# Kernel tuning notes

Measured on AMD Instinct MI355X. Metric: run time of the kernel, lower is better.

The kernel has to match this reference:

```python
import jax, jax.numpy as jnp
import numpy as np

B, SEQ_LEN, N_VARS, N_MARK = 16, 96, 862, 4
D_MODEL, D_STATE, D_CONV, D_FF = 512, 16, 2, 512
DT_RANK = 32  # ceil(d_model/16)
E_LAYERS = 2
PRED_LEN = 96
EPS = 1e-5


def _layer_norm(x, w, b):
    mu = x.mean(-1, keepdims=True)
    var = ((x - mu) ** 2).mean(-1, keepdims=True)
    return (x - mu) / jnp.sqrt(var + EPS) * w + b


def _selective_scan(xc, dt, Bm, Cm, A, D):
    # xc, dt: [B,S,d]; Bm, Cm: [B,S,ds]; A: [d,ds]; D: [d]
    def step(h, inp):
        x_t, dt_t, B_t, C_t = inp  # [B,d],[B,d],[B,ds],[B,ds]
        dA = jnp.exp(dt_t[..., None] * A)                      # [B,d,ds]
        h = dA * h + (dt_t * x_t)[..., None] * B_t[:, None, :]
        return h, jnp.einsum('bds,bs->bd', h, C_t)
    h0 = jnp.zeros((xc.shape[0], A.shape[0], A.shape[1]), xc.dtype)
    xs = tuple(jnp.swapaxes(t, 0, 1) for t in (xc, dt, Bm, Cm))
    _, ys = jax.lax.scan(step, h0, xs)
    return jnp.swapaxes(ys, 0, 1) + xc * D


def _mamba(x, in_W, conv_W, conv_b, xproj_W, dt_W, dt_b, A_log, D, out_W):
    d = in_W.shape[0] // 2
    xz = x @ in_W.T                                             # [B,S,2d]
    xi, z = xz[..., :d], xz[..., d:]
    xp = jnp.pad(xi, ((0, 0), (1, 0), (0, 0)))                  # causal pad, d_conv=2
    xc = xp[:, :-1] * conv_W[:, 0] + xp[:, 1:] * conv_W[:, 1] + conv_b
    xc = jax.nn.silu(xc)
    dbc = xc @ xproj_W.T                                        # [B,S,dt_rank+2*ds]
    dtr = dbc[..., :DT_RANK]
    Bm = dbc[..., DT_RANK:DT_RANK + D_STATE]
    Cm = dbc[..., DT_RANK + D_STATE:]
    dt = jax.nn.softplus(dtr @ dt_W.T + dt_b)
    A = -jnp.exp(A_log)
    y = _selective_scan(xc, dt, Bm, Cm, A, D)
    return (y * jax.nn.silu(z)) @ out_W.T


def _forward(x_enc, x_mark_enc, emb_W, emb_b,
             mf_in_W, mf_conv_W, mf_conv_b, mf_xproj_W, mf_dt_W, mf_dt_b, mf_A_log, mf_D, mf_out_W,
             mr_in_W, mr_conv_W, mr_conv_b, mr_xproj_W, mr_dt_W, mr_dt_b, mr_A_log, mr_D, mr_out_W,
             conv1_W, conv1_b, conv2_W, conv2_b, ln1_w, ln1_b, ln2_w, ln2_b,
             enc_norm_w, enc_norm_b, proj_W, proj_b):
    # RevIN-style instance normalization over time
    means = x_enc.mean(1, keepdims=True)
    xe = x_enc - means
    stdev = jnp.sqrt(jnp.mean(xe ** 2, axis=1, keepdims=True) + EPS)  # unbiased=False
    xe = xe / stdev
    N = x_enc.shape[2]
    # inverted embedding: variates (+ time marks) are tokens, Linear over time axis
    tok = jnp.concatenate([jnp.swapaxes(xe, 1, 2), jnp.swapaxes(x_mark_enc, 1, 2)], axis=1)
    x = tok @ emb_W.T + emb_b                                   # [B, N+4, d_model]
    for l in range(E_LAYERS):
        fwd = _mamba(x, mf_in_W[l], mf_conv_W[l], mf_conv_b[l], mf_xproj_W[l],
                     mf_dt_W[l], mf_dt_b[l], mf_A_log[l], mf_D[l], mf_out_W[l])
        rev = _mamba(x[:, ::-1], mr_in_W[l], mr_conv_W[l], mr_conv_b[l], mr_xproj_W[l],
                     mr_dt_W[l], mr_dt_b[l], mr_A_log[l], mr_D[l], mr_out_W[l])[:, ::-1]
        x = x + fwd + rev
        y = x = _layer_norm(x, ln1_w[l], ln1_b[l])
        y = jax.nn.relu(y @ conv1_W[l].T + conv1_b[l])          # 1x1 conv == linear
        y = y @ conv2_W[l].T + conv2_b[l]
        x = _layer_norm(x + y, ln2_w[l], ln2_b[l])
    x = _layer_norm(x, enc_norm_w, enc_norm_b)
    dec = jnp.swapaxes(x @ proj_W.T + proj_b, 1, 2)[:, :, :N]   # [B, pred_len, N]
    dec = dec * stdev[:, 0][:, None, :] + means[:, 0][:, None, :]
    return dec


def setup_inputs() -> dict:
    key = jax.random.key(0)
    ks = iter(jax.random.split(key, 64))
    nrm = lambda shape, s=0.02: jax.random.normal(next(ks), shape, jnp.float32) * s
    inp = {
        'x_enc': jax.random.normal(next(ks), (B, SEQ_LEN, N_VARS), jnp.float32),
        'x_mark_enc': jax.random.normal(next(ks), (B, SEQ_LEN, N_MARK), jnp.float32),
        'x_dec': jnp.zeros((1, 1, 1), jnp.float32),
        'x_mark_dec': jnp.zeros((1, 1, 1), jnp.float32),
        'emb_W': nrm((D_MODEL, SEQ_LEN)),
        'emb_b': jnp.zeros((D_MODEL,), jnp.float32),
    }
    for p in ('mf', 'mr'):
        inp[p + '_in_W'] = nrm((E_LAYERS, 2 * D_MODEL, D_MODEL))
        inp[p + '_conv_W'] = nrm((E_LAYERS, D_MODEL, D_CONV), 0.1)
        inp[p + '_conv_b'] = jnp.zeros((E_LAYERS, D_MODEL), jnp.float32)
        inp[p + '_xproj_W'] = nrm((E_LAYERS, DT_RANK + 2 * D_STATE, D_MODEL))
        inp[p + '_dt_W'] = nrm((E_LAYERS, D_MODEL, DT_RANK), 0.1)
        inp[p + '_dt_b'] = nrm((E_LAYERS, D_MODEL), 0.1)
        inp[p + '_A_log'] = jnp.log(jnp.broadcast_to(
            jnp.arange(1, D_STATE + 1, dtype=jnp.float32), (E_LAYERS, D_MODEL, D_STATE)))
        inp[p + '_D'] = jnp.ones((E_LAYERS, D_MODEL), jnp.float32)
        inp[p + '_out_W'] = nrm((E_LAYERS, D_MODEL, D_MODEL))
    inp['conv1_W'] = nrm((E_LAYERS, D_FF, D_MODEL))
    inp['conv1_b'] = jnp.zeros((E_LAYERS, D_FF), jnp.float32)
    inp['conv2_W'] = nrm((E_LAYERS, D_MODEL, D_FF))
    inp['conv2_b'] = jnp.zeros((E_LAYERS, D_MODEL), jnp.float32)
    inp['ln1_w'] = jnp.ones((E_LAYERS, D_MODEL), jnp.float32)
    inp['ln1_b'] = jnp.zeros((E_LAYERS, D_MODEL), jnp.float32)
    inp['ln2_w'] = jnp.ones((E_LAYERS, D_MODEL), jnp.float32)
    inp['ln2_b'] = jnp.zeros((E_LAYERS, D_MODEL), jnp.float32)
    inp['enc_norm_w'] = jnp.ones((D_MODEL,), jnp.float32)
    inp['enc_norm_b'] = jnp.zeros((D_MODEL,), jnp.float32)
    inp['proj_W'] = nrm((PRED_LEN, D_MODEL))
    inp['proj_b'] = jnp.zeros((PRED_LEN,), jnp.float32)
    return inp


def reference(x_enc, x_mark_enc, x_dec, x_mark_dec, emb_W, emb_b,
              mf_in_W, mf_conv_W, mf_conv_b, mf_xproj_W, mf_dt_W, mf_dt_b, mf_A_log, mf_D, mf_out_W,
              mr_in_W, mr_conv_W, mr_conv_b, mr_xproj_W, mr_dt_W, mr_dt_b, mr_A_log, mr_D, mr_out_W,
              conv1_W, conv1_b, conv2_W, conv2_b, ln1_w, ln1_b, ln2_w, ln2_b,
              enc_norm_w, enc_norm_b, proj_W, proj_b):
    return _forward(x_enc, x_mark_enc, emb_W, emb_b,
                    mf_in_W, mf_conv_W, mf_conv_b, mf_xproj_W, mf_dt_W, mf_dt_b, mf_A_log, mf_D, mf_out_W,
                    mr_in_W, mr_conv_W, mr_conv_b, mr_xproj_W, mr_dt_W, mr_dt_b, mr_A_log, mr_D, mr_out_W,
                    conv1_W, conv1_b, conv2_W, conv2_b, ln1_w, ln1_b, ln2_w, ln2_b,
                    enc_norm_w, enc_norm_b, proj_W, proj_b)
```

## Files before the change

kernel.cpp:

```cpp
#include <hip/hip_runtime.h>
#include <math.h>

#define BATCH   16
#define SEQ     96
#define NVARS   862
#define NMARK   4
#define LTOK    866
#define MROWS   (BATCH*LTOK)
#define DM      512
#define DSTATE  16
#define DTRANK  32
#define DFF     512
#define PRED    96
#define EPS_F   1e-5f

#define CCH     32
#define TCH     28

typedef __attribute__((ext_vector_type(4))) float f32x4;
typedef __attribute__((ext_vector_type(8))) short bf16x8;

#define LDSK 40

__device__ __forceinline__ short f2bf(float f) {
    unsigned u = __builtin_bit_cast(unsigned, f);
    u += 0x7fffu + ((u >> 16) & 1u);
    return (short)(u >> 16);
}

__global__ __launch_bounds__(256) void gemm_mfma(
    const float* __restrict__ A, int lda,
    const float* __restrict__ W,
    const float* __restrict__ bias,
    const float* __restrict__ res,
    float* __restrict__ out, int ldo,
    int M, int N, int K, int rev, int act,
    int final_mode, const float* __restrict__ fstd, const float* __restrict__ fmean)
{
    __shared__ short Als[128 * LDSK];
    __shared__ short Bls[128 * LDSK];
    const int tid  = threadIdx.x;
    const int lane = tid & 63;
    const int wid  = tid >> 6;
    const int wm   = wid >> 1;
    const int wn   = wid & 1;
    const int fr   = lane & 15;
    const int g    = lane >> 4;
    const int m0 = blockIdx.y * 128, n0 = blockIdx.x * 128;

    int    rowq[4], kgq[4];
    size_t aoff[4], woff[4];
    bool   aval[4], wval[4];
#pragma unroll
    for (int q = 0; q < 4; ++q) {
        const int slot = tid + q * 256;
        const int row = slot >> 3, kg = slot & 7;
        rowq[q] = row; kgq[q] = kg;
        const int gm = m0 + row;
        aval[q] = (gm < M);
        int rm = gm;
        if (rev && aval[q]) { int b = gm / LTOK; int t = gm - b * LTOK; rm = b * LTOK + (LTOK - 1 - t); }
        aoff[q] = (size_t)rm * lda + kg * 4;
        const int gn = n0 + row;
        wval[q] = (gn < N);
        woff[q] = (size_t)gn * K + kg * 4;
    }

    f32x4 acc[4][4];
#pragma unroll
    for (int i = 0; i < 4; ++i)
#pragma unroll
        for (int j = 0; j < 4; ++j) { f32x4 z = {0.f, 0.f, 0.f, 0.f}; acc[i][j] = z; }

    for (int k0 = 0; k0 < K; k0 += 32) {
        float4 avq[4], wvq[4];
        const float4 f0 = make_float4(0.f, 0.f, 0.f, 0.f);
#pragma unroll
        for (int q = 0; q < 4; ++q) {
            avq[q] = aval[q] ? *(const float4*)(A + aoff[q] + k0) : f0;
            wvq[q] = wval[q] ? *(const float4*)(W + woff[q] + k0) : f0;
        }
        __syncthreads();
#pragma unroll
        for (int q = 0; q < 4; ++q) {
            short4 sa, sw;
            sa.x = f2bf(avq[q].x); sa.y = f2bf(avq[q].y);
            sa.z = f2bf(avq[q].z); sa.w = f2bf(avq[q].w);
            sw.x = f2bf(wvq[q].x); sw.y = f2bf(wvq[q].y);
            sw.z = f2bf(wvq[q].z); sw.w = f2bf(wvq[q].w);
            *(short4*)&Als[rowq[q] * LDSK + kgq[q] * 4] = sa;
            *(short4*)&Bls[rowq[q] * LDSK + kgq[q] * 4] = sw;
        }
        __syncthreads();

        bf16x8 a4[4], b4[4];
#pragma unroll
        for (int i = 0; i < 4; ++i) {
            a4[i] = *(const bf16x8*)&Als[(wm * 64 + i * 16 + fr) * LDSK + g * 8];
            b4[i] = *(const bf16x8*)&Bls[(wn * 64 + i * 16 + fr) * LDSK + g * 8];
        }
#pragma unroll
        for (int mi = 0; mi < 4; ++mi)
#pragma unroll
            for (int ni = 0; ni < 4; ++ni)
                acc[mi][ni] = __builtin_amdgcn_mfma_f32_16x16x32_bf16(
                    a4[mi], b4[ni], acc[mi][ni], 0, 0, 0);
    }

#pragma unroll
    for (int mi = 0; mi < 4; ++mi) {
#pragma unroll
        for (int ni = 0; ni < 4; ++ni) {
            const int gn = n0 + wn * 64 + ni * 16 + fr;
            if (gn >= N) continue;
#pragma unroll
            for (int j = 0; j < 4; ++j) {
                const int gm = m0 + wm * 64 + mi * 16 + g * 4 + j;
                if (gm >= M) continue;
                float v = acc[mi][ni][j];
                if (bias) v += bias[gn];
                if (act == 1) v = fmaxf(v, 0.f);
                else if (act == 2) v = (v > 20.f) ? v : log1pf(__expf(v));
                if (res) v += res[(size_t)gm * DM + gn];
                if (!final_mode) {
                    out[(size_t)gm * ldo + gn] = v;
                } else {
                    const int bb = gm / LTOK, vv = gm - bb * LTOK;
                    if (vv < NVARS) {
                        out[((size_t)bb * PRED + gn) * NVARS + vv] =
                            v * fstd[bb * NVARS + vv] + fmean[bb * NVARS + vv];
                    }
                }
            }
        }
    }
}

__global__ void stats_kernel(const float* __restrict__ x_enc,
                             float* __restrict__ means, float* __restrict__ stdev)
{
    int i = blockIdx.x * blockDim.x + threadIdx.x;
    if (i >= BATCH * NVARS) return;
    int b = i / NVARS, v = i - b * NVARS;
    const float* p = x_enc + (size_t)b * SEQ * NVARS + v;
    float s = 0.f;
    for (int t = 0; t < SEQ; ++t) s += p[(size_t)t * NVARS];
    float mu = s / (float)SEQ;
    float ss = 0.f;
    for (int t = 0; t < SEQ; ++t) { float d = p[(size_t)t * NVARS] - mu; ss += d * d; }
    means[i] = mu;
    stdev[i] = sqrtf(ss / (float)SEQ + EPS_F);
}

__global__ void tok_kernel(const float* __restrict__ x_enc, const float* __restrict__ x_mark,
                           const float* __restrict__ means, const float* __restrict__ stdev,
                           float* __restrict__ tok)
{
    int i = blockIdx.x * blockDim.x + threadIdx.x;
    if (i >= MROWS * SEQ) return;
    int s = i % SEQ;
    int row = i / SEQ;
    int b = row / LTOK, l = row - b * LTOK;
    float val;
    if (l < NVARS) {
        val = (x_enc[((size_t)b * SEQ + s) * NVARS + l] - means[b * NVARS + l])
              / stdev[b * NVARS + l];
    } else {
        val = x_mark[((size_t)b * SEQ + s) * NMARK + (l - NVARS)];
    }
    tok[i] = val;
}

__global__ void conv_silu_kernel(const float* __restrict__ xz, float* __restrict__ xc,
                                 const float* __restrict__ cW, const float* __restrict__ cb)
{
    int i = blockIdx.x * blockDim.x + threadIdx.x;
    if (i >= MROWS * DM) return;
    int d = i & (DM - 1);
    int row = i >> 9;
    int t = row % LTOK;
    float cur = xz[(size_t)row * 1024 + d];
    float prev = (t == 0) ? 0.f : xz[(size_t)(row - 1) * 1024 + d];
    float v = prev * cW[d * 2 + 0] + cur * cW[d * 2 + 1] + cb[d];
    xc[i] = v * (1.f / (1.f + __expf(-v)));
}

__global__ __launch_bounds__(256) void scan1_kernel(
    const float* __restrict__ xc, const float* __restrict__ dt,
    const float* __restrict__ dbc, const float* __restrict__ A_log,
    float* __restrict__ aprod, float* __restrict__ hpart)
{
    __shared__ float Ls[TCH * 32];
    const int tid = threadIdx.x;
    const int d = blockIdx.x * 256 + tid;
    const int c = blockIdx.y;
    const int b = blockIdx.z;
    const int t0 = c * TCH;
    const int tend = min(t0 + TCH, LTOK);
    const size_t rowb = (size_t)b * LTOK;

    for (int i = tid; i < TCH * 32; i += 256) {
        const int tr = min(t0 + (i >> 5), LTOK - 1);
        Ls[i] = dbc[(rowb + tr) * 64 + 32 + (i & 31)];
    }
    __syncthreads();

    float Ads[16];
#pragma unroll
    for (int s = 0; s < 16; ++s) Ads[s] = -__expf(A_log[d * DSTATE + s]);
    float h[16];
#pragma unroll
    for (int s = 0; s < 16; ++s) h[s] = 0.f;
    float sumdt = 0.f;

    for (int t = t0; t < tend; ++t) {
        const size_t row = rowb + t;
        const float dtv = dt[row * DM + d];
        const float xcv = xc[row * DM + d];
        const float du = dtv * xcv;
        sumdt += dtv;
        const float* Bp = &Ls[(t - t0) * 32];
#pragma unroll
        for (int s = 0; s < 16; ++s) {
            const float dA = __expf(dtv * Ads[s]);
            h[s] = dA * h[s] + du * Bp[s];
        }
    }
#pragma unroll
    for (int s = 0; s < 16; ++s) {
        const size_t oidx = ((size_t)(b * CCH + c) * 16 + s) * DM + d;
        aprod[oidx] = __expf(Ads[s] * sumdt);
        hpart[oidx] = h[s];
    }
}

__global__ __launch_bounds__(256) void scan2_kernel(
    const float* __restrict__ aprod, const float* __restrict__ hpart,
    float* __restrict__ hinit)
{
    const int gid = blockIdx.x * 256 + threadIdx.x;
    const int d = gid & (DM - 1);
    const int s = (gid >> 9) & 15;
    const int b = gid >> 13;
    float h = 0.f;
    for (int c = 0; c < CCH; ++c) {
        const size_t idx = ((size_t)(b * CCH + c) * 16 + s) * DM + d;
        const float ap = aprod[idx];
        const float hp = hpart[idx];
        hinit[idx] = h;
        h = hp + ap * h;
    }
}

__global__ __launch_bounds__(256) void scan3_kernel(
    const float* __restrict__ xc, const float* __restrict__ dt,
    const float* __restrict__ dbc, const float* __restrict__ xz,
    const float* __restrict__ A_log, const float* __restrict__ Dp,
    const float* __restrict__ hinit, float* __restrict__ ym)
{
    __shared__ float Ls[TCH * 32];
    const int tid = threadIdx.x;
    const int d = blockIdx.x * 256 + tid;
    const int c = blockIdx.y;
    const int b = blockIdx.z;
    const int t0 = c * TCH;
    const int tend = min(t0 + TCH, LTOK);
    const size_t rowb = (size_t)b * LTOK;

    for (int i = tid; i < TCH * 32; i += 256) {
        const int tr = min(t0 + (i >> 5), LTOK - 1);
        Ls[i] = dbc[(rowb + tr) * 64 + 32 + (i & 31)];
    }
    __syncthreads();

    float Ads[16];
#pragma unroll
    for (int s = 0; s < 16; ++s) Ads[s] = -__expf(A_log[d * DSTATE + s]);
    float h[16];
#pragma unroll
    for (int s = 0; s < 16; ++s)
        h[s] = hinit[((size_t)(b * CCH + c) * 16 + s) * DM + d];
    const float Dd = Dp[d];

    for (int t = t0; t < tend; ++t) {
        const size_t row = rowb + t;
        const float dtv = dt[row * DM + d];
        const float xcv = xc[row * DM + d];
        const float du = dtv * xcv;
        const float* Bp = &Ls[(t - t0) * 32];
        float p0 = 0.f, p1 = 0.f, p2 = 0.f, p3 = 0.f;
#pragma unroll
        for (int s = 0; s < 16; ++s) {
            const float dA = __expf(dtv * Ads[s]);
            const float hn = dA * h[s] + du * Bp[s];
            h[s] = hn;
            const float pc = hn * Bp[16 + s];
            if ((s & 3) == 0) p0 += pc;
            else if ((s & 3) == 1) p1 += pc;
            else if ((s & 3) == 2) p2 += pc;
            else p3 += pc;
        }
        const float y = (p0 + p1) + (p2 + p3) + xcv * Dd;
        const float z = xz[row * 1024 + DM + d];
        ym[row * DM + d] = y * (z * (1.f / (1.f + __expf(-z))));
    }
}

__global__ __launch_bounds__(256) void ln_kernel(const float* __restrict__ in,
                                                 const float* __restrict__ w,
                                                 const float* __restrict__ bp,
                                                 float* __restrict__ out)
{
    const int row = blockIdx.x;
    const int tid = threadIdx.x;
    const float2 v = *(const float2*)(in + (size_t)row * DM + tid * 2);
    float s  = v.x + v.y;
    float ss = v.x * v.x + v.y * v.y;
    for (int off = 32; off; off >>= 1) {
        s  += __shfl_down(s, off);
        ss += __shfl_down(ss, off);
    }
    __shared__ float sh[10];
    const int wid = tid >> 6, lane = tid & 63;
    if (lane == 0) { sh[wid] = s; sh[4 + wid] = ss; }
    __syncthreads();
    if (tid == 0) {
        float S = sh[0] + sh[1] + sh[2] + sh[3];
        float SS = sh[4] + sh[5] + sh[6] + sh[7];
        float mu = S / (float)DM;
        float var = SS / (float)DM - mu * mu;
        sh[8] = mu; sh[9] = rsqrtf(var + EPS_F);
    }
    __syncthreads();
    const float mu = sh[8], rstd = sh[9];
    const int c = tid * 2;
    float2 o;
    o.x = (v.x - mu) * rstd * w[c]     + bp[c];
    o.y = (v.y - mu) * rstd * w[c + 1] + bp[c + 1];
    *(float2*)(out + (size_t)row * DM + c) = o;
}

static inline void launch_gemm(hipStream_t st, const float* A, int lda, const float* W,
                               const float* bias, const float* res, float* out, int ldo,
                               int M, int N, int K, int rev, int act,
                               int fin = 0, const float* fstd = nullptr, const float* fmean = nullptr)
{
    dim3 g((N + 127) / 128, (M + 127) / 128);
    hipLaunchKernelGGL(gemm_mfma, g, dim3(256), 0, st,
                       A, lda, W, bias, res, out, ldo, M, N, K, rev, act, fin, fstd, fmean);
}

extern "C" void kernel_launch(void* const* d_in, const int* in_sizes, int n_in,
                              void* d_out, int out_size, void* d_ws, size_t ws_size,
                              hipStream_t stream)
{
    const float* x_enc   = (const float*)d_in[0];
    const float* x_mark  = (const float*)d_in[1];
    const float* emb_W   = (const float*)d_in[4];
    const float* emb_b   = (const float*)d_in[5];
    const float* m_in_W[2]    = { (const float*)d_in[6],  (const float*)d_in[15] };
    const float* m_conv_W[2]  = { (const float*)d_in[7],  (const float*)d_in[16] };
    const float* m_conv_b[2]  = { (const float*)d_in[8],  (const float*)d_in[17] };
    const float* m_xproj_W[2] = { (const float*)d_in[9],  (const float*)d_in[18] };
    const float* m_dt_W[2]    = { (const float*)d_in[10], (const float*)d_in[19] };
    const float* m_dt_b[2]    = { (const float*)d_in[11], (const float*)d_in[20] };
    const float* m_A_log[2]   = { (const float*)d_in[12], (const float*)d_in[21] };
    const float* m_D[2]       = { (const float*)d_in[13], (const float*)d_in[22] };
    const float* m_out_W[2]   = { (const float*)d_in[14], (const float*)d_in[23] };
    const float* conv1_W = (const float*)d_in[24];
    const float* conv1_b = (const float*)d_in[25];
    const float* conv2_W = (const float*)d_in[26];
    const float* conv2_b = (const float*)d_in[27];
    const float* ln1_w = (const float*)d_in[28];
    const float* ln1_b = (const float*)d_in[29];
    const float* ln2_w = (const float*)d_in[30];
    const float* ln2_b = (const float*)d_in[31];
    const float* enc_w = (const float*)d_in[32];
    const float* enc_b = (const float*)d_in[33];
    const float* proj_W = (const float*)d_in[34];
    const float* proj_b = (const float*)d_in[35];

    float* ws = (float*)d_ws;
    size_t o = 0;
    float* means = ws + o; o += 13824;
    float* stdev = ws + o; o += 13824;
    float* xbuf  = ws + o; o += (size_t)MROWS * DM;
    float* accb  = ws + o; o += (size_t)MROWS * DM;
    float* xzb   = ws + o; o += (size_t)MROWS * 1024;
    float* xcb   = ws + o; o += (size_t)MROWS * DM;
    float* dtb   = ws + o; o += (size_t)MROWS * DM;
    float* dbcb  = ws + o; o += (size_t)MROWS * 64;
    float* ybuf  = ws + o; o += (size_t)MROWS * DM;
    const size_t NSUM = (size_t)BATCH * CCH * 16 * DM;
    float* aprod = ws + o; o += NSUM;
    float* hpart = ws + o; o += NSUM;
    float* hinit = ws + o; o += NSUM;
    float* tok   = xzb;
    float* hbuf  = xzb;
    float* x2buf = ybuf;

    hipLaunchKernelGGL(stats_kernel, dim3((BATCH * NVARS + 255) / 256), dim3(256), 0, stream,
                       x_enc, means, stdev);
    hipLaunchKernelGGL(tok_kernel, dim3((MROWS * SEQ + 255) / 256), dim3(256), 0, stream,
                       x_enc, x_mark, means, stdev, tok);
    launch_gemm(stream, tok, SEQ, emb_W, emb_b, nullptr, xbuf, DM, MROWS, DM, SEQ, 0, 0);

    for (int l = 0; l < 2; ++l) {
        for (int dir = 0; dir < 2; ++dir) {
            const float* inW  = m_in_W[dir]    + (size_t)l * 2 * DM * DM;
            const float* cW   = m_conv_W[dir]  + (size_t)l * DM * 2;
            const float* cb   = m_conv_b[dir]  + (size_t)l * DM;
            const float* xpW  = m_xproj_W[dir] + (size_t)l * 64 * DM;
            const float* dtW  = m_dt_W[dir]    + (size_t)l * DM * DTRANK;
            const float* dtbias = m_dt_b[dir]  + (size_t)l * DM;
            const float* Alog = m_A_log[dir]   + (size_t)l * DM * DSTATE;
            const float* Dp   = m_D[dir]       + (size_t)l * DM;
            const float* outW = m_out_W[dir]   + (size_t)l * DM * DM;

            launch_gemm(stream, xbuf, DM, inW, nullptr, nullptr, xzb, 1024,
                        MROWS, 2 * DM, DM, dir, 0);
            hipLaunchKernelGGL(conv_silu_kernel, dim3((MROWS * DM + 255) / 256), dim3(256),
                               0, stream, xzb, xcb, cW, cb);
            launch_gemm(stream, xcb, DM, xpW, nullptr, nullptr, dbcb, 64,
                        MROWS, 64, DM, 0, 0);
            launch_gemm(stream, dbcb, 64, dtW, dtbias, nullptr, dtb, DM,
                        MROWS, DM, DTRANK, 0, 2);
            hipLaunchKernelGGL(scan1_kernel, dim3(2, CCH, BATCH), dim3(256), 0, stream,
                               xcb, dtb, dbcb, Alog, aprod, hpart);
            hipLaunchKernelGGL(scan2_kernel, dim3((BATCH * 16 * DM) / 256), dim3(256), 0, stream,
                               aprod, hpart, hinit);
            hipLaunchKernelGGL(scan3_kernel, dim3(2, CCH, BATCH), dim3(256), 0, stream,
                               xcb, dtb, dbcb, xzb, Alog, Dp, hinit, ybuf);
            launch_gemm(stream, ybuf, DM, outW, nullptr, dir == 0 ? xbuf : accb,
                        accb, DM, MROWS, DM, DM, dir, 0);
        }
        hipLaunchKernelGGL(ln_kernel, dim3(MROWS), dim3(256), 0, stream,
                           accb, ln1_w + l * DM, ln1_b + l * DM, x2buf);
        launch_gemm(stream, x2buf, DM, conv1_W + (size_t)l * DFF * DM,
                    conv1_b + l * DFF, nullptr, hbuf, DFF, MROWS, DFF, DM, 0, 1);
        launch_gemm(stream, hbuf, DFF, conv2_W + (size_t)l * DM * DFF,
                    conv2_b + l * DM, x2buf, accb, DM, MROWS, DM, DFF, 0, 0);
        hipLaunchKernelGGL(ln_kernel, dim3(MROWS), dim3(256), 0, stream,
                           accb, ln2_w + l * DM, ln2_b + l * DM, xbuf);
    }

    hipLaunchKernelGGL(ln_kernel, dim3(MROWS), dim3(256), 0, stream,
                       xbuf, enc_w, enc_b, x2buf);
    launch_gemm(stream, x2buf, DM, proj_W, proj_b, nullptr, (float*)d_out, 0,
                MROWS, PRED, DM, 0, 0, 1, stdev, means);
}
```

Baseline: 1.785 ms.

## Store GEMM operands as bf16 and load tiles directly into LDS

```diff
diff --git a/kernel.cpp b/kernel.cpp
--- a/kernel.cpp
+++ b/kernel.cpp
@@ -19,51 +19,57 @@
 
 typedef __attribute__((ext_vector_type(4))) float f32x4;
 typedef __attribute__((ext_vector_type(8))) short bf16x8;
-
-#define LDSK 40
+typedef unsigned short ushort_t;
 
 __device__ __forceinline__ short f2bf(float f) {
     unsigned u = __builtin_bit_cast(unsigned, f);
     u += 0x7fffu + ((u >> 16) & 1u);
     return (short)(u >> 16);
 }
-
-__global__ __launch_bounds__(256) void gemm_mfma(
-    const float* __restrict__ A, int lda,
-    const float* __restrict__ W,
+__device__ __forceinline__ float bf2f(ushort_t u) {
+    return __builtin_bit_cast(float, (unsigned)u << 16);
+}
+
+__device__ __forceinline__ void gl2lds16(const ushort_t* g, ushort_t* l) {
+    __builtin_amdgcn_global_load_lds(
+        (const __attribute__((address_space(1))) unsigned int*)(g),
+        (__attribute__((address_space(3))) unsigned int*)(l),
+        16, 0, 0);
+}
+
+__global__ __launch_bounds__(256) void gemm_bf16(
+    const ushort_t* __restrict__ A, int lda,
+    const ushort_t* __restrict__ W, int ldw,
     const float* __restrict__ bias,
-    const float* __restrict__ res,
-    float* __restrict__ out, int ldo,
-    int M, int N, int K, int rev, int act,
-    int final_mode, const float* __restrict__ fstd, const float* __restrict__ fmean)
-{
-    __shared__ short Als[128 * LDSK];
-    __shared__ short Bls[128 * LDSK];
+    const float* __restrict__ resf, const ushort_t* __restrict__ resb,
+    float* __restrict__ outf, ushort_t* __restrict__ outb, int ldo,
+    int M, int N, int K, int rev, int act, int mode,
+    const float* __restrict__ fstd, const float* __restrict__ fmean)
+{
+    __shared__ ushort_t Als[128 * 32];
+    __shared__ ushort_t Bls[128 * 32];
     const int tid  = threadIdx.x;
     const int lane = tid & 63;
-    const int wid  = tid >> 6;
-    const int wm   = wid >> 1;
-    const int wn   = wid & 1;
-    const int fr   = lane & 15;
-    const int g    = lane >> 4;
+    const int w    = tid >> 6;
+    const int wm   = w >> 1;
+    const int wn   = w & 1;
     const int m0 = blockIdx.y * 128, n0 = blockIdx.x * 128;
 
-    int    rowq[4], kgq[4];
-    size_t aoff[4], woff[4];
-    bool   aval[4], wval[4];
-#pragma unroll
-    for (int q = 0; q < 4; ++q) {
-        const int slot = tid + q * 256;
-        const int row = slot >> 3, kg = slot & 7;
-        rowq[q] = row; kgq[q] = kg;
-        const int gm = m0 + row;
-        aval[q] = (gm < M);
+    size_t asrc[2], wsrc[2];
+    int lbase[2];
+#pragma unroll
+    for (int i = 0; i < 2; ++i) {
+        const int byte = (i * 4 + w) * 1024 + lane * 16;
+        const int row  = byte >> 6;
+        const int c    = (byte >> 4) & 3;
+        const int g    = c ^ ((row >> 1) & 3);
+        int gm = m0 + row; if (gm > M - 1) gm = M - 1;
         int rm = gm;
-        if (rev && aval[q]) { int b = gm / LTOK; int t = gm - b * LTOK; rm = b * LTOK + (LTOK - 1 - t); }
-        aoff[q] = (size_t)rm * lda + kg * 4;
-        const int gn = n0 + row;
-        wval[q] = (gn < N);
-        woff[q] = (size_t)gn * K + kg * 4;
+        if (rev) { int b = gm / LTOK; int t = gm - b * LTOK; rm = b * LTOK + (LTOK - 1 - t); }
+        asrc[i] = (size_t)rm * lda + g * 8;
+        int gn = n0 + row; if (gn > N - 1) gn = N - 1;
+        wsrc[i] = (size_t)gn * ldw + g * 8;
+        lbase[i] = (i * 4 + w) * 512;
     }
 
     f32x4 acc[4][4];
@@ -72,32 +78,23 @@
 #pragma unroll
         for (int j = 0; j < 4; ++j) { f32x4 z = {0.f, 0.f, 0.f, 0.f}; acc[i][j] = z; }
 
+    const int fr = lane & 15;
+    const int kg = lane >> 4;
+    const int cg = kg ^ ((fr >> 1) & 3);
+
     for (int k0 = 0; k0 < K; k0 += 32) {
-        float4 avq[4], wvq[4];
-        const float4 f0 = make_float4(0.f, 0.f, 0.f, 0.f);
-#pragma unroll
-        for (int q = 0; q < 4; ++q) {
-            avq[q] = aval[q] ? *(const float4*)(A + aoff[q] + k0) : f0;
-            wvq[q] = wval[q] ? *(const float4*)(W + woff[q] + k0) : f0;
-        }
         __syncthreads();
-#pragma unroll
-        for (int q = 0; q < 4; ++q) {
-            short4 sa, sw;
-            sa.x = f2bf(avq[q].x); sa.y = f2bf(avq[q].y);
-            sa.z = f2bf(avq[q].z); sa.w = f2bf(avq[q].w);
-            sw.x = f2bf(wvq[q].x); sw.y = f2bf(wvq[q].y);
-            sw.z = f2bf(wvq[q].z); sw.w = f2bf(wvq[q].w);
-            *(short4*)&Als[rowq[q] * LDSK + kgq[q] * 4] = sa;
-            *(short4*)&Bls[rowq[q] * LDSK + kgq[q] * 4] = sw;
-        }
+        gl2lds16(A + asrc[0] + k0, &Als[lbase[0]]);
+        gl2lds16(A + asrc[1] + k0, &Als[lbase[1]]);
+        gl2lds16(W + wsrc[0] + k0, &Bls[lbase[0]]);
+        gl2lds16(W + wsrc[1] + k0, &Bls[lbase[1]]);
         __syncthreads();
 
         bf16x8 a4[4], b4[4];
 #pragma unroll
         for (int i = 0; i < 4; ++i) {
-            a4[i] = *(const bf16x8*)&Als[(wm * 64 + i * 16 + fr) * LDSK + g * 8];
-            b4[i] = *(const bf16x8*)&Bls[(wn * 64 + i * 16 + fr) * LDSK + g * 8];
+            a4[i] = *(const bf16x8*)&Als[(wm * 64 + i * 16 + fr) * 32 + cg * 8];
+            b4[i] = *(const bf16x8*)&Bls[(wn * 64 + i * 16 + fr) * 32 + cg * 8];
         }
 #pragma unroll
         for (int mi = 0; mi < 4; ++mi)
@@ -115,25 +112,44 @@
             if (gn >= N) continue;
 #pragma unroll
             for (int j = 0; j < 4; ++j) {
-                const int gm = m0 + wm * 64 + mi * 16 + g * 4 + j;
+                const int gm = m0 + wm * 64 + mi * 16 + kg * 4 + j;
                 if (gm >= M) continue;
                 float v = acc[mi][ni][j];
                 if (bias) v += bias[gn];
                 if (act == 1) v = fmaxf(v, 0.f);
                 else if (act == 2) v = (v > 20.f) ? v : log1pf(__expf(v));
-                if (res) v += res[(size_t)gm * DM + gn];
-                if (!final_mode) {
-                    out[(size_t)gm * ldo + gn] = v;
+                if (resf) v += resf[(size_t)gm * DM + gn];
+                else if (resb) v += bf2f(resb[(size_t)gm * DM + gn]);
+                if (mode == 0) {
+                    if (outf) outf[(size_t)gm * ldo + gn] = v;
+                    if (outb) outb[(size_t)gm * ldo + gn] = (ushort_t)f2bf(v);
+                } else if (mode == 2) {
+                    if (gn < DM) outf[(size_t)gm * DM + gn] = v;
+                    else         outb[(size_t)gm * DM + gn - DM] = (ushort_t)f2bf(v);
                 } else {
                     const int bb = gm / LTOK, vv = gm - bb * LTOK;
                     if (vv < NVARS) {
-                        out[((size_t)bb * PRED + gn) * NVARS + vv] =
+                        outf[((size_t)bb * PRED + gn) * NVARS + vv] =
                             v * fstd[bb * NVARS + vv] + fmean[bb * NVARS + vv];
                     }
                 }
             }
         }
     }
+}
+
+struct CvtJobs {
+    const float* src[12];
+    ushort_t*    dst[12];
+    int          n[12];
+};
+__global__ void cvt_kernel(CvtJobs jobs) {
+    const int j = blockIdx.y;
+    const float* s = jobs.src[j];
+    ushort_t* d = jobs.dst[j];
+    const int n = jobs.n[j];
+    for (int i = blockIdx.x * blockDim.x + threadIdx.x; i < n; i += gridDim.x * blockDim.x)
+        d[i] = (ushort_t)f2bf(s[i]);
 }
 
 __global__ void stats_kernel(const float* __restrict__ x_enc,
@@ -154,7 +170,7 @@
 
 __global__ void tok_kernel(const float* __restrict__ x_enc, const float* __restrict__ x_mark,
                            const float* __restrict__ means, const float* __restrict__ stdev,
-                           float* __restrict__ tok)
+                           ushort_t* __restrict__ tok)
 {
     int i = blockIdx.x * blockDim.x + threadIdx.x;
     if (i >= MROWS * SEQ) return;
@@ -168,10 +184,11 @@
     } else {
         val = x_mark[((size_t)b * SEQ + s) * NMARK + (l - NVARS)];
     }
-    tok[i] = val;
-}
-
-__global__ void conv_silu_kernel(const float* __restrict__ xz, float* __restrict__ xc,
+    tok[i] = (ushort_t)f2bf(val);
+}
+
+__global__ void conv_silu_kernel(const float* __restrict__ xi, float* __restrict__ xc,
+                                 ushort_t* __restrict__ xc_bf,
                                  const float* __restrict__ cW, const float* __restrict__ cb)
 {
     int i = blockIdx.x * blockDim.x + threadIdx.x;
@@ -179,10 +196,12 @@
     int d = i & (DM - 1);
     int row = i >> 9;
     int t = row % LTOK;
-    float cur = xz[(size_t)row * 1024 + d];
-    float prev = (t == 0) ? 0.f : xz[(size_t)(row - 1) * 1024 + d];
+    float cur = xi[i];
+    float prev = (t == 0) ? 0.f : xi[i - DM];
     float v = prev * cW[d * 2 + 0] + cur * cW[d * 2 + 1] + cb[d];
-    xc[i] = v * (1.f / (1.f + __expf(-v)));
+    float sv = v * (1.f / (1.f + __expf(-v)));
+    xc[i] = sv;
+    xc_bf[i] = (ushort_t)f2bf(sv);
 }
 
 __global__ __launch_bounds__(256) void scan1_kernel(
@@ -235,8 +254,7 @@
 }
 
 __global__ __launch_bounds__(256) void scan2_kernel(
-    const float* __restrict__ aprod, const float* __restrict__ hpart,
-    float* __restrict__ hinit)
+    float* __restrict__ aprod, const float* __restrict__ hpart)
 {
     const int gid = blockIdx.x * 256 + threadIdx.x;
     const int d = gid & (DM - 1);
@@ -247,16 +265,16 @@
         const size_t idx = ((size_t)(b * CCH + c) * 16 + s) * DM + d;
         const float ap = aprod[idx];
         const float hp = hpart[idx];
-        hinit[idx] = h;
+        aprod[idx] = h;
         h = hp + ap * h;
     }
 }
 
 __global__ __launch_bounds__(256) void scan3_kernel(
     const float* __restrict__ xc, const float* __restrict__ dt,
-    const float* __restrict__ dbc, const float* __restrict__ xz,
+    const float* __restrict__ dbc, const ushort_t* __restrict__ zbf,
     const float* __restrict__ A_log, const float* __restrict__ Dp,
-    const float* __restrict__ hinit, float* __restrict__ ym)
+    const float* __restrict__ hinit, ushort_t* __restrict__ ym)
 {
     __shared__ float Ls[TCH * 32];
     const int tid = threadIdx.x;
@@ -301,15 +319,16 @@
             else p3 += pc;
         }
         const float y = (p0 + p1) + (p2 + p3) + xcv * Dd;
-        const float z = xz[row * 1024 + DM + d];
-        ym[row * DM + d] = y * (z * (1.f / (1.f + __expf(-z))));
+        const float z = bf2f(zbf[row * DM + d]);
+        ym[row * DM + d] = (ushort_t)f2bf(y * (z * (1.f / (1.f + __expf(-z)))));
     }
 }
 
 __global__ __launch_bounds__(256) void ln_kernel(const float* __restrict__ in,
                                                  const float* __restrict__ w,
                                                  const float* __restrict__ bp,
-                                                 float* __restrict__ out)
+                                                 float* __restrict__ outf,
+                                                 ushort_t* __restrict__ outb)
 {
     const int row = blockIdx.x;
     const int tid = threadIdx.x;
@@ -337,17 +356,24 @@
     float2 o;
     o.x = (v.x - mu) * rstd * w[c]     + bp[c];
     o.y = (v.y - mu) * rstd * w[c + 1] + bp[c + 1];
-    *(float2*)(out + (size_t)row * DM + c) = o;
-}
-
-static inline void launch_gemm(hipStream_t st, const float* A, int lda, const float* W,
-                               const float* bias, const float* res, float* out, int ldo,
-                               int M, int N, int K, int rev, int act,
-                               int fin = 0, const float* fstd = nullptr, const float* fmean = nullptr)
+    if (outf) *(float2*)(outf + (size_t)row * DM + c) = o;
+    if (outb) {
+        unsigned pk = (unsigned)(ushort_t)f2bf(o.x) | ((unsigned)(ushort_t)f2bf(o.y) << 16);
+        ((unsigned*)outb)[(size_t)row * (DM / 2) + tid] = pk;
+    }
+}
+
+static inline void launch_gemm(hipStream_t st, const ushort_t* A, int lda,
+                               const ushort_t* W, int ldw, const float* bias,
+                               const float* resf, const ushort_t* resb,
+                               float* outf, ushort_t* outb, int ldo,
+                               int M, int N, int K, int rev, int act, int mode = 0,
+                               const float* fstd = nullptr, const float* fmean = nullptr)
 {
     dim3 g((N + 127) / 128, (M + 127) / 128);
-    hipLaunchKernelGGL(gemm_mfma, g, dim3(256), 0, st,
-                       A, lda, W, bias, res, out, ldo, M, N, K, rev, act, fin, fstd, fmean);
+    hipLaunchKernelGGL(gemm_bf16, g, dim3(256), 0, st,
+                       A, lda, W, ldw, bias, resf, resb, outf, outb, ldo,
+                       M, N, K, rev, act, mode, fstd, fmean);
 }
 
 extern "C" void kernel_launch(void* const* d_in, const int* in_sizes, int n_in,
@@ -380,72 +406,106 @@
     const float* proj_W = (const float*)d_in[34];
     const float* proj_b = (const float*)d_in[35];
 
+    const size_t MD = (size_t)MROWS * DM;
     float* ws = (float*)d_ws;
     size_t o = 0;
     float* means = ws + o; o += 13824;
     float* stdev = ws + o; o += 13824;
-    float* xbuf  = ws + o; o += (size_t)MROWS * DM;
-    float* accb  = ws + o; o += (size_t)MROWS * DM;
-    float* xzb   = ws + o; o += (size_t)MROWS * 1024;
-    float* xcb   = ws + o; o += (size_t)MROWS * DM;
-    float* dtb   = ws + o; o += (size_t)MROWS * DM;
+    float* xbuf  = ws + o; o += MD;
+    float* accb  = ws + o; o += MD;
+    float* xib   = ws + o; o += MD;
+    float* xcb   = ws + o; o += MD;
+    float* dtb   = ws + o; o += MD;
     float* dbcb  = ws + o; o += (size_t)MROWS * 64;
-    float* ybuf  = ws + o; o += (size_t)MROWS * DM;
-    const size_t NSUM = (size_t)BATCH * CCH * 16 * DM;
-    float* aprod = ws + o; o += NSUM;
-    float* hpart = ws + o; o += NSUM;
-    float* hinit = ws + o; o += NSUM;
-    float* tok   = xzb;
-    float* hbuf  = xzb;
-    float* x2buf = ybuf;
+    float* hpart = ws + o; o += (size_t)BATCH * CCH * 16 * DM;
+    float* aprod = xib;
+    float* x2f   = xib;
+
+    ushort_t* wsb = (ushort_t*)(ws + o);
+    size_t so = 0;
+    ushort_t* xbuf_bf = wsb + so; so += MD;
+    ushort_t* xcb_bf  = wsb + so; so += MD;
+    ushort_t* ybuf_bf = wsb + so; so += MD;
+    ushort_t* x2_bf   = wsb + so; so += MD;
+    ushort_t* zbf     = wsb + so; so += MD;
+    ushort_t* dbcb_bf = wsb + so; so += (size_t)MROWS * 64;
+    ushort_t* embW_bf = wsb + so; so += 49152;
+    ushort_t* inW_bf[2];  inW_bf[0] = wsb + so; so += 1048576; inW_bf[1] = wsb + so; so += 1048576;
+    ushort_t* xpW_bf[2];  xpW_bf[0] = wsb + so; so += 65536;   xpW_bf[1] = wsb + so; so += 65536;
+    ushort_t* dtW_bf[2];  dtW_bf[0] = wsb + so; so += 32768;   dtW_bf[1] = wsb + so; so += 32768;
+    ushort_t* outW_bf[2]; outW_bf[0] = wsb + so; so += 524288; outW_bf[1] = wsb + so; so += 524288;
+    ushort_t* c1W_bf = wsb + so; so += 524288;
+    ushort_t* c2W_bf = wsb + so; so += 524288;
+    ushort_t* projW_bf = wsb + so; so += 49152;
+    ushort_t* tok_bf = x2_bf;
+    ushort_t* hbuf_bf = ybuf_bf;
+
+    CvtJobs jobs;
+    jobs.src[0] = emb_W;      jobs.dst[0] = embW_bf;    jobs.n[0] = 49152;
+    jobs.src[1] = m_in_W[0];  jobs.dst[1] = inW_bf[0];  jobs.n[1] = 1048576;
+    jobs.src[2] = m_in_W[1];  jobs.dst[2] = inW_bf[1];  jobs.n[2] = 1048576;
+    jobs.src[3] = m_xproj_W[0]; jobs.dst[3] = xpW_bf[0]; jobs.n[3] = 65536;
+    jobs.src[4] = m_xproj_W[1]; jobs.dst[4] = xpW_bf[1]; jobs.n[4] = 65536;
+    jobs.src[5] = m_dt_W[0];  jobs.dst[5] = dtW_bf[0];  jobs.n[5] = 32768;
+    jobs.src[6] = m_dt_W[1];  jobs.dst[6] = dtW_bf[1];  jobs.n[6] = 32768;
+    jobs.src[7] = m_out_W[0]; jobs.dst[7] = outW_bf[0]; jobs.n[7] = 524288;
+    jobs.src[8] = m_out_W[1]; jobs.dst[8] = outW_bf[1]; jobs.n[8] = 524288;
+    jobs.src[9] = conv1_W;    jobs.dst[9] = c1W_bf;     jobs.n[9] = 524288;
+    jobs.src[10] = conv2_W;   jobs.dst[10] = c2W_bf;    jobs.n[10] = 524288;
+    jobs.src[11] = proj_W;    jobs.dst[11] = projW_bf;  jobs.n[11] = 49152;
+    hipLaunchKernelGGL(cvt_kernel, dim3(64, 12), dim3(256), 0, stream, jobs);
 
     hipLaunchKernelGGL(stats_kernel, dim3((BATCH * NVARS + 255) / 256), dim3(256), 0, stream,
                        x_enc, means, stdev);
     hipLaunchKernelGGL(tok_kernel, dim3((MROWS * SEQ + 255) / 256), dim3(256), 0, stream,
-                       x_enc, x_mark, means, stdev, tok);
-    launch_gemm(stream, tok, SEQ, emb_W, emb_b, nullptr, xbuf, DM, MROWS, DM, SEQ, 0, 0);
+                       x_enc, x_mark, means, stdev, tok_bf);
+    launch_gemm(stream, tok_bf, SEQ, embW_bf, SEQ, emb_b, nullptr, nullptr,
+                xbuf, xbuf_bf, DM, MROWS, DM, SEQ, 0, 0);
 
     for (int l = 0; l < 2; ++l) {
         for (int dir = 0; dir < 2; ++dir) {
-            const float* inW  = m_in_W[dir]    + (size_t)l * 2 * DM * DM;
+            const ushort_t* inW  = inW_bf[dir]  + (size_t)l * 2 * DM * DM;
             const float* cW   = m_conv_W[dir]  + (size_t)l * DM * 2;
             const float* cb   = m_conv_b[dir]  + (size_t)l * DM;
-            const float* xpW  = m_xproj_W[dir] + (size_t)l * 64 * DM;
-            const float* dtW  = m_dt_W[dir]    + (size_t)l * DM * DTRANK;
+            const ushort_t* xpW  = xpW_bf[dir] + (size_t)l * 64 * DM;
+            const ushort_t* dtW  = dtW_bf[dir] + (size_t)l * DM * DTRANK;
             const float* dtbias = m_dt_b[dir]  + (size_t)l * DM;
             const float* Alog = m_A_log[dir]   + (size_t)l * DM * DSTATE;
             const float* Dp   = m_D[dir]       + (size_t)l * DM;
-            const float* outW = m_out_W[dir]   + (size_t)l * DM * DM;
-
-            launch_gemm(stream, xbuf, DM, inW, nullptr, nullptr, xzb, 1024,
-                        MROWS, 2 * DM, DM, dir, 0);
+            const ushort_t* outW = outW_bf[dir] + (size_t)l * DM * DM;
+
+            launch_gemm(stream, xbuf_bf, DM, inW, DM, nullptr, nullptr, nullptr,
+                        xib, zbf, 0, MROWS, 2 * DM, DM, dir, 0, 2);
             hipLaunchKernelGGL(conv_silu_kernel, dim3((MROWS * DM + 255) / 256), dim3(256),
-                               0, stream, xzb, xcb, cW, cb);
-            launch_gemm(stream, xcb, DM, xpW, nullptr, nullptr, dbcb, 64,
-                        MROWS, 64, DM, 0, 0);
-            launch_gemm(stream, dbcb, 64, dtW, dtbias, nullptr, dtb, DM,
-                        MROWS, DM, DTRANK, 0, 2);
+                               0, stream, xib, xcb, xcb_bf, cW, cb);
+            launch_gemm(stream, xcb_bf, DM, xpW, DM, nullptr, nullptr, nullptr,
+                        dbcb, dbcb_bf, 64, MROWS, 64, DM, 0, 0);
+            launch_gemm(stream, dbcb_bf, 64, dtW, DTRANK, dtbias, nullptr, nullptr,
+                        dtb, nullptr, DM, MROWS, DM, DTRANK, 0, 2);
             hipLaunchKernelGGL(scan1_kernel, dim3(2, CCH, BATCH), dim3(256), 0, stream,
                                xcb, dtb, dbcb, Alog, aprod, hpart);
             hipLaunchKernelGGL(scan2_kernel, dim3((BATCH * 16 * DM) / 256), dim3(256), 0, stream,
-                               aprod, hpart, hinit);
+                               aprod, hpart);
             hipLaunchKernelGGL(scan3_kernel, dim3(2, CCH, BATCH), dim3(256), 0, stream,
-                               xcb, dtb, dbcb, xzb, Alog, Dp, hinit, ybuf);
-            launch_gemm(stream, ybuf, DM, outW, nullptr, dir == 0 ? xbuf : accb,
-                        accb, DM, MROWS, DM, DM, dir, 0);
+                               xcb, dtb, dbcb, zbf, Alog, Dp, aprod, ybuf_bf);
+            launch_gemm(stream, ybuf_bf, DM, outW, DM, nullptr,
+                        dir == 0 ? xbuf : accb, nullptr,
+                        accb, nullptr, DM, MROWS, DM, DM, dir, 0);
         }
         hipLaunchKernelGGL(ln_kernel, dim3(MROWS), dim3(256), 0, stream,
-                           accb, ln1_w + l * DM, ln1_b + l * DM, x2buf);
-        launch_gemm(stream, x2buf, DM, conv1_W + (size_t)l * DFF * DM,
-                    conv1_b + l * DFF, nullptr, hbuf, DFF, MROWS, DFF, DM, 0, 1);
-        launch_gemm(stream, hbuf, DFF, conv2_W + (size_t)l * DM * DFF,
-                    conv2_b + l * DM, x2buf, accb, DM, MROWS, DM, DFF, 0, 0);
+                           accb, ln1_w + l * DM, ln1_b + l * DM, x2f, x2_bf);
+        launch_gemm(stream, x2_bf, DM, c1W_bf + (size_t)l * DFF * DM, DM,
+                    conv1_b + l * DFF, nullptr, nullptr,
+                    nullptr, hbuf_bf, DFF, MROWS, DFF, DM, 0, 1);
+        launch_gemm(stream, hbuf_bf, DFF, c2W_bf + (size_t)l * DM * DFF, DFF,
+                    conv2_b + l * DM, x2f, nullptr,
+                    accb, nullptr, DM, MROWS, DM, DFF, 0, 0);
         hipLaunchKernelGGL(ln_kernel, dim3(MROWS), dim3(256), 0, stream,
-                           accb, ln2_w + l * DM, ln2_b + l * DM, xbuf);
+                           accb, ln2_w + l * DM, ln2_b + l * DM, xbuf, xbuf_bf);
     }
 
     hipLaunchKernelGGL(ln_kernel, dim3(MROWS), dim3(256), 0, stream,
-                       xbuf, enc_w, enc_b, x2buf);
-    launch_gemm(stream, x2buf, DM, proj_W, proj_b, nullptr, (float*)d_out, 0,
-                MROWS, PRED, DM, 0, 0, 1, stdev, means);
-}
+                       xbuf, enc_w, enc_b, nullptr, x2_bf);
+    launch_gemm(stream, x2_bf, DM, projW_bf, DM, proj_b, nullptr, nullptr,
+                (float*)d_out, nullptr, 0, MROWS, PRED, DM, 0, 0, 1, stdev, means);
+}
```

Result: slower. 3.179 ms (+78.2%).
